# Optimization experiments

Hardware: AMD Instinct MI355X
Metric: run time of the kernel (lower is better)

## Reference

```python
import jax, jax.numpy as jnp
import numpy as np

HEADS = 8
HDIM = 64
MAX_PEMB = 512


def setup_inputs() -> dict:
    key = jax.random.key(0)
    ks = jax.random.split(key, 6)
    B, S, D = 4, 1024, 512
    return {
        "x": jax.random.normal(ks[0], (B, S, D), jnp.float32),
        "attn_mask": jnp.ones((B, S), jnp.bool_),
        "Wq": jax.random.normal(ks[1], (D, HEADS * HDIM), jnp.float32) * 0.02,
        "Wkv": jax.random.normal(ks[2], (D, 2 * HEADS * HDIM), jnp.float32) * 0.02,
        "Wout": jax.random.normal(ks[3], (HEADS * HDIM, D), jnp.float32) * 0.02,
        "bout": jnp.zeros((D,), jnp.float32),
        "pemb": jax.random.normal(ks[4], (2 * MAX_PEMB + 1, HDIM), jnp.float32) * 0.02,
    }


def reference(x, attn_mask, Wq, Wkv, Wout, bout, pemb):
    # attn_mask is unpacked but unused in the original call(); faithful to source.
    B, S, D = x.shape
    scale = HDIM ** (-0.5)

    q = (x @ Wq).reshape(B, S, HEADS, HDIM).transpose(0, 2, 1, 3)  # [B,H,S,hd]
    kv = x @ Wkv
    k, v = jnp.split(kv, 2, axis=-1)
    k = k.reshape(B, S, HEADS, HDIM).transpose(0, 2, 1, 3)
    v = v.reshape(B, S, HEADS, HDIM).transpose(0, 2, 1, 3)

    attn_score = jnp.einsum('bhqd,bhkd->bhqk', q, k) * scale

    seq = jnp.arange(S)
    dist = jnp.clip(seq[:, None] - seq[None, :], -MAX_PEMB, MAX_PEMB) + MAX_PEMB  # [S,S]
    rel_pemb = pemb[dist]  # [S,S,hd]
    pos_attn = jnp.einsum('bhsd,std->bhst', q, rel_pemb) * scale  # [B,H,S,S]

    attn_probs = jax.nn.softmax(attn_score + pos_attn, axis=-1)
    ctx = jnp.einsum('bhqk,bhkd->bqhd', attn_probs, v).reshape(B, S, HEADS * HDIM)
    return ctx @ Wout + bout
```

## Files before the change

kernel.cpp:

```cpp
#include <hip/hip_runtime.h>
#include <hip/hip_bf16.h>

constexpr int BATCH = 4;
constexpr int SEQ   = 1024;
constexpr int DM    = 512;
constexpr int NH    = 8;
constexpr int HD    = 64;
constexpr int NQKV  = 1536;

typedef unsigned short u16;
typedef __attribute__((ext_vector_type(8))) __bf16 bf8;
typedef __attribute__((ext_vector_type(4))) __bf16 bf4;
typedef __attribute__((ext_vector_type(4))) float  f4;
typedef __attribute__((ext_vector_type(16))) float f16v;

#define MFMA16(a, b, c) __builtin_amdgcn_mfma_f32_16x16x32_bf16(a, b, c, 0, 0, 0)
#define MFMA32(a, b, c) __builtin_amdgcn_mfma_f32_32x32x16_bf16(a, b, c, 0, 0, 0)

#define QSC 0.18033688f

static __device__ __forceinline__ u16 f2b(float f) {
    union { float f; unsigned u; } v; v.f = f;
    unsigned r = v.u + 0x7FFFu + ((v.u >> 16) & 1u);
    return (u16)(r >> 16);
}
static __device__ __forceinline__ float b2f(u16 x) {
    union { unsigned u; float f; } v; v.u = (unsigned)x << 16;
    return v.f;
}
static __device__ __forceinline__ float fexp2(float x) {
    return __builtin_amdgcn_exp2f(x);
}
static __device__ __forceinline__ void gl_lds16(const void* g, void* l) {
    __builtin_amdgcn_global_load_lds(
        (const __attribute__((address_space(1))) void*)g,
        (__attribute__((address_space(3))) void*)l, 16, 0, 0);
}
static __device__ __forceinline__ unsigned cvtpk_bf16(float lo, float hi) {
    unsigned r;
    asm("v_cvt_pk_bf16_f32 %0, %1, %2" : "=v"(r) : "v"(lo), "v"(hi));
    return r;
}
static __device__ __forceinline__ void swap32(unsigned &a, unsigned &b) {
    asm("v_permlane32_swap_b32 %0, %1" : "+v"(a), "+v"(b));
}

__device__ __forceinline__ void tcvt_tile(const float* __restrict__ in,
                                          u16* __restrict__ out,
                                          int R, int C, int bx, int by, int tid,
                                          float (*t)[33]) {
    int r0 = by * 32, c0 = bx * 32;
    int lc = tid & 31, lr = tid >> 5;
    #pragma unroll
    for (int p = 0; p < 4; p++) {
        int r = lr + p * 8;
        t[r][lc] = in[(size_t)(r0 + r) * C + c0 + lc];
    }
    __syncthreads();
    #pragma unroll
    for (int p = 0; p < 4; p++) {
        int r = lr + p * 8;
        out[(size_t)(c0 + r) * R + r0 + lc] = f2b(t[lc][r]);
    }
}

__global__ __launch_bounds__(256)
void prep(const float* __restrict__ x, const float* __restrict__ Wq,
          const float* __restrict__ Wkv, const float* __restrict__ Wout,
          const float* __restrict__ pemb,
          u16* __restrict__ xb, u16* __restrict__ qkvw,
          u16* __restrict__ Woutt, u16* __restrict__ pembb) {
    __shared__ float t[32][33];
    const int blk = blockIdx.x, tid = threadIdx.x;
    if (blk < 2048) {
        int i = (blk * 256 + tid) * 4;
        float4 v = *(const float4*)(x + i);
        ushort4 o = {f2b(v.x), f2b(v.y), f2b(v.z), f2b(v.w)};
        *(ushort4*)(xb + i) = o;
    } else if (blk < 2113) {
        int i = ((blk - 2048) * 256 + tid) * 4;
        if (i < 1025 * HD) {
            float4 v = *(const float4*)(pemb + i);
            ushort4 o = {f2b(v.x), f2b(v.y), f2b(v.z), f2b(v.w)};
            *(ushort4*)(pembb + i) = o;
        }
    } else if (blk < 2369) {
        int l = blk - 2113;
        tcvt_tile(Wq, qkvw, 512, 512, l & 15, l >> 4, tid, t);
    } else if (blk < 2881) {
        int l = blk - 2369;
        tcvt_tile(Wkv, qkvw + 512 * 512, 512, 1024, l & 31, l >> 5, tid, t);
    } else {
        int l = blk - 2881;
        tcvt_tile(Wout, Woutt, 512, 512, l & 15, l >> 4, tid, t);
    }
}

template<int BN>
__global__ __launch_bounds__(256)
void gemm_bt(const u16* __restrict__ A, const u16* __restrict__ Bt,
             int M, int N, int K,
             float* __restrict__ Cf, const float* __restrict__ bias,
             __bf16* __restrict__ qtb, __bf16* __restrict__ ktb,
             __bf16* __restrict__ vtb) {
    constexpr int NJ = BN / 32;
    __shared__ __align__(16) u16 As[2][64][32];
    __shared__ __align__(16) u16 Bs[2][BN][32];
    const int tid = threadIdx.x, w = tid >> 6, lane = tid & 63;
    const int l15 = lane & 15, l4 = lane >> 4;
    const int wr = (w >> 1) * 32, wc = (w & 1) * (BN / 2);
    const int bm = blockIdx.y * 64, bn = blockIdx.x * BN;

    f4 acc[2][NJ];
    #pragma unroll
    for (int i = 0; i < 2; i++)
        #pragma unroll
        for (int j = 0; j < NJ; j++) acc[i][j] = (f4){0.f, 0.f, 0.f, 0.f};

    const int rS = lane >> 2;
    const int cS = (lane & 3) * 8;

    for (int k0 = 0; k0 < K; k0 += 64) {
        #pragma unroll
        for (int ks = 0; ks < 2; ks++) {
            gl_lds16(A + (size_t)(bm + w * 16 + rS) * K + k0 + ks * 32 + cS,
                     &As[ks][w * 16][0]);
            #pragma unroll
            for (int rb = 0; rb < BN / 4; rb += 16)
                gl_lds16(Bt + (size_t)(bn + w * (BN / 4) + rb + rS) * K
                             + k0 + ks * 32 + cS,
                         &Bs[ks][w * (BN / 4) + rb][0]);
        }
        __syncthreads();
        #pragma unroll
        for (int ks = 0; ks < 2; ks++) {
            bf8 af[2], bf[NJ];
            #pragma unroll
            for (int i = 0; i < 2; i++)
                af[i] = *(const bf8*)&As[ks][wr + i * 16 + l15][l4 * 8];
            #pragma unroll
            for (int j = 0; j < NJ; j++)
                bf[j] = *(const bf8*)&Bs[ks][wc + j * 16 + l15][l4 * 8];
            #pragma unroll
            for (int i = 0; i < 2; i++)
                #pragma unroll
                for (int j = 0; j < NJ; j++)
                    acc[i][j] = MFMA16(af[i], bf[j], acc[i][j]);
        }
        __syncthreads();
    }
    #pragma unroll
    for (int i = 0; i < 2; i++)
        #pragma unroll
        for (int j = 0; j < NJ; j++) {
            const int col = bn + wc + j * 16 + l15;
            const int row0 = bm + wr + i * 16 + l4 * 4;
            if (Cf) {
                #pragma unroll
                for (int reg = 0; reg < 4; reg++)
                    Cf[(size_t)(row0 + reg) * N + col] = acc[i][j][reg] + bias[col];
            } else if (col < 512) {
                int h = col >> 6, d = col & 63;
                #pragma unroll
                for (int reg = 0; reg < 4; reg++) {
                    int row = row0 + reg;
                    int b = row >> 10, t = row & 1023;
                    qtb[((((size_t)(b * 8 + h)) << 10 | t) << 6) | d] =
                        (__bf16)(acc[i][j][reg] * QSC);
                }
            } else if (col < 1024) {
                int h = (col >> 6) - 8, d = col & 63;
                #pragma unroll
                for (int reg = 0; reg < 4; reg++) {
                    int row = row0 + reg;
                    int b = row >> 10, t = row & 1023;
                    ktb[((((size_t)(b * 8 + h)) << 10 | t) << 6) | d] =
                        (__bf16)acc[i][j][reg];
                }
            } else {
                int h = (col >> 6) - 16, d = col & 63;
                int b = row0 >> 10, t = row0 & 1023;
                __bf16 pk[4];
                #pragma unroll
                for (int reg = 0; reg < 4; reg++) pk[reg] = (__bf16)acc[i][j][reg];
                *(ushort4*)&vtb[(((size_t)(b * 8 + h) * 64 + d) << 10) | t] =
                    *(ushort4*)pk;
            }
        }
}

__global__ __launch_bounds__(256)
void attn_mfma(const u16* __restrict__ qtb, const u16* __restrict__ ktb,
               const u16* __restrict__ vtb, const u16* __restrict__ pembb,
               __bf16* __restrict__ ctxb) {
    __shared__ __align__(16) __bf16 Kb[2][64][72];
    __shared__ __align__(16) __bf16 Vb[2][64][72];
    __shared__ __align__(16) __bf16 Qd[256][72];

    const int tid = threadIdx.x, w = tid >> 6, lane = tid & 63;
    const int l31 = lane & 31, hi = lane >> 5;
    const int wq = w >> 1, wt = w & 1;
    const int bh = blockIdx.x, b = bh >> 3;
    const int s0 = blockIdx.y * 64;

    bf8 qb[4];
    {
        const u16* qp = qtb + ((size_t)bh * SEQ + s0 + wq * 32 + l31) * HD + hi * 8;
        #pragma unroll
        for (int st = 0; st < 4; st++) qb[st] = *(const bf8*)(qp + st * 16);
    }

    #pragma unroll
    for (int pass = 0; pass < 2; pass++) {
        const int jr = s0 + 449 + pass * 64 + wt * 32 + l31;
        const int jc = min(1024, max(0, jr));
        const u16* pp = pembb + (size_t)jc * HD + hi * 8;
        f16v acc;
        #pragma unroll
        for (int r = 0; r < 16; r++) acc[r] = 0.f;
        #pragma unroll
        for (int st = 0; st < 4; st++) {
            bf8 pj = *(const bf8*)(pp + st * 16);
            acc = MFMA32(qb[st], pj, acc);
        }
        #pragma unroll
        for (int o4 = 0; o4 < 4; o4++) {
            bf4 pk;
            #pragma unroll
            for (int r = 0; r < 4; r++) pk[r] = (__bf16)acc[o4 * 4 + r];
            *(bf4*)&Qd[jr & 255][wq * 32 + o4 * 8 + hi * 4] = pk;
        }
    }

    float l_lane = 0.f;
    f16v oo[2];
    #pragma unroll
    for (int dt = 0; dt < 2; dt++)
        #pragma unroll
        for (int r = 0; r < 16; r++) oo[dt][r] = 0.f;

    const u16* kbase = ktb + (size_t)bh * SEQ * HD;
    const u16* vbase = vtb + (size_t)bh * HD * SEQ;
    const int sr = tid >> 3, sc = (tid & 7) * 8;

    *(bf8*)&Kb[0][sr][sc]      = *(const bf8*)(kbase + (size_t)sr * HD + sc);
    *(bf8*)&Kb[0][sr + 32][sc] = *(const bf8*)(kbase + (size_t)(sr + 32) * HD + sc);
    *(bf8*)&Vb[0][sr][sc]      = *(const bf8*)(vbase + (size_t)sr * SEQ + sc);
    *(bf8*)&Vb[0][sr + 32][sc] = *(const bf8*)(vbase + (size_t)(sr + 32) * SEQ + sc);
    __syncthreads();

    for (int i = 0; i < 16; i++) {
        const int cur = i & 1, nxt = cur ^ 1;
        const int t0 = i * 64, t1 = t0 + 64;
        const bool pre = (i < 15);
        bf8 kr0, kr1, vr0, vr1, pj0, pj1, pj2, pj3;
        const int jrn = s0 + 449 - 64 * (i + 1) + wt * 32 + l31;
        if (pre) {
            kr0 = *(const bf8*)(kbase + (size_t)(t1 + sr) * HD + sc);
            kr1 = *(const bf8*)(kbase + (size_t)(t1 + sr + 32) * HD + sc);
            vr0 = *(const bf8*)(vbase + (size_t)sr * SEQ + t1 + sc);
            vr1 = *(const bf8*)(vbase + (size_t)(sr + 32) * SEQ + t1 + sc);
            const int jc = min(1024, max(0, jrn));
            const u16* pp = pembb + (size_t)jc * HD + hi * 8;
            pj0 = *(const bf8*)(pp);
            pj1 = *(const bf8*)(pp + 16);
            pj2 = *(const bf8*)(pp + 32);
            pj3 = *(const bf8*)(pp + 48);
        }

        bf8 ka[4];
        #pragma unroll
        for (int st = 0; st < 4; st++)
            ka[st] = *(const bf8*)&Kb[cur][wt * 32 + l31][st * 16 + hi * 8];
        const int jcst = (s0 - t0 + 512) + wq * 32 + l31 - wt * 32 - 4 * hi;
        const u16* qdc = (const u16*)&Qd[0][0] + wq * 32 + l31;
        u16 rg[16];
        #pragma unroll
        for (int r = 0; r < 16; r++) {
            const int pat = (r & 3) + 8 * (r >> 2);
            rg[r] = qdc[((jcst - pat) & 255) * 72];
        }
        bf8 vf00 = *(const bf8*)&Vb[cur][l31][wt * 32 + hi * 8];
        bf8 vf01 = *(const bf8*)&Vb[cur][l31][wt * 32 + 16 + hi * 8];
        bf8 vf10 = *(const bf8*)&Vb[cur][32 + l31][wt * 32 + hi * 8];
        bf8 vf11 = *(const bf8*)&Vb[cur][32 + l31][wt * 32 + 16 + hi * 8];

        __builtin_amdgcn_s_setprio(1);
        f16v s16;
        #pragma unroll
        for (int r = 0; r < 16; r++) s16[r] = 0.f;
        #pragma unroll
        for (int st = 0; st < 4; st++) s16 = MFMA32(ka[st], qb[st], s16);
        __builtin_amdgcn_s_setprio(0);

        float p[16];
        float la = 0.f, lb = 0.f;
        #pragma unroll
        for (int r = 0; r < 8; r++) {
            float pv = fexp2(s16[r] + b2f(rg[r]));
            p[r] = pv; la += pv;
        }
        unsigned w00 = cvtpk_bf16(p[0], p[1]), w01 = cvtpk_bf16(p[2], p[3]);
        unsigned w10 = cvtpk_bf16(p[4], p[5]), w11 = cvtpk_bf16(p[6], p[7]);
        swap32(w00, w10); swap32(w01, w11);
        union { unsigned u[4]; bf8 v; } pa0, pa1;
        pa0.u[0] = w00; pa0.u[1] = w01; pa0.u[2] = w10; pa0.u[3] = w11;
        __builtin_amdgcn_s_setprio(1);
        oo[0] = MFMA32(pa0.v, vf00, oo[0]);
        oo[1] = MFMA32(pa0.v, vf10, oo[1]);
        __builtin_amdgcn_s_setprio(0);

        if (pre) {
            *(bf8*)&Kb[nxt][sr][sc]      = kr0;
            *(bf8*)&Kb[nxt][sr + 32][sc] = kr1;
            *(bf8*)&Vb[nxt][sr][sc]      = vr0;
            *(bf8*)&Vb[nxt][sr + 32][sc] = vr1;
        }
        f16v rf;
        if (pre) {
            #pragma unroll
            for (int r = 0; r < 16; r++) rf[r] = 0.f;
            rf = MFMA32(qb[0], pj0, rf);
            rf = MFMA32(qb[1], pj1, rf);
            rf = MFMA32(qb[2], pj2, rf);
            rf = MFMA32(qb[3], pj3, rf);
        }

        #pragma unroll
        for (int r = 8; r < 16; r++) {
            float pv = fexp2(s16[r] + b2f(rg[r]));
            p[r] = pv; lb += pv;
        }
        unsigned w20 = cvtpk_bf16(p[8],  p[9]),  w21 = cvtpk_bf16(p[10], p[11]);
        unsigned w30 = cvtpk_bf16(p[12], p[13]), w31 = cvtpk_bf16(p[14], p[15]);
        swap32(w20, w30); swap32(w21, w31);
        pa1.u[0] = w20; pa1.u[1] = w21; pa1.u[2] = w30; pa1.u[3] = w31;
        __builtin_amdgcn_s_setprio(1);
        oo[0] = MFMA32(pa1.v, vf01, oo[0]);
        oo[1] = MFMA32(pa1.v, vf11, oo[1]);
        __builtin_amdgcn_s_setprio(0);
        l_lane += la + lb;

        if (pre) {
            #pragma unroll
            for (int o4 = 0; o4 < 4; o4++) {
                bf4 pk;
                #pragma unroll
                for (int r = 0; r < 4; r++) pk[r] = (__bf16)rf[o4 * 4 + r];
                *(bf4*)&Qd[jrn & 255][wq * 32 + o4 * 8 + hi * 4] = pk;
            }
        }
        __syncthreads();
    }

    float lsum = l_lane + __shfl_xor(l_lane, 32);
    float* Os = (float*)&Qd[0][0];
    float* Ls = Os + 4096;
    if (lane < 32) Ls[(wq * 2 + wt) * 32 + l31] = lsum;
    if (wt == 0) {
        #pragma unroll
        for (int dt = 0; dt < 2; dt++)
            #pragma unroll
            for (int r = 0; r < 16; r++) {
                const int q = (r & 3) + 8 * (r >> 2) + 4 * hi;
                Os[(wq * 32 + q) * 64 + dt * 32 + l31] = oo[dt][r];
            }
    }
    __syncthreads();
    if (wt == 1) {
        const int h = bh & 7;
        #pragma unroll
        for (int r = 0; r < 16; r++) {
            const int q = (r & 3) + 8 * (r >> 2) + 4 * hi;
            const float li = 1.f / (Ls[wq * 64 + q] + Ls[wq * 64 + 32 + q]);
            #pragma unroll
            for (int dt = 0; dt < 2; dt++) {
                float v = (oo[dt][r] + Os[(wq * 32 + q) * 64 + dt * 32 + l31]) * li;
                ctxb[(size_t)(b * SEQ + s0 + wq * 32 + q) * DM + h * HD + dt * 32 + l31]
                    = (__bf16)v;
            }
        }
    }
}

extern "C" void kernel_launch(void* const* d_in, const int* in_sizes, int n_in,
                              void* d_out, int out_size, void* d_ws, size_t ws_size,
                              hipStream_t stream) {
    const float* x    = (const float*)d_in[0];
    const float* Wq   = (const float*)d_in[2];
    const float* Wkv  = (const float*)d_in[3];
    const float* Wout = (const float*)d_in[4];
    const float* bout = (const float*)d_in[5];
    const float* pemb = (const float*)d_in[6];
    float* out = (float*)d_out;

    const int M = BATCH * SEQ;
    u16* p = (u16*)d_ws;
    u16* xb    = p; p += (size_t)M * DM;
    u16* qkvw  = p; p += (size_t)NQKV * DM;
    u16* Woutt = p; p += (size_t)DM * DM;
    u16* pembb = p; p += (size_t)1025 * HD;
    u16* qtb   = p; p += (size_t)M * DM;
    u16* ktb   = p; p += (size_t)M * DM;
    u16* vtb   = p; p += (size_t)M * DM;
    u16* ctxb  = p; p += (size_t)M * DM;

    prep<<<3137, 256, 0, stream>>>(x, Wq, Wkv, Wout, pemb, xb, qkvw, Woutt, pembb);

    gemm_bt<128><<<dim3(NQKV / 128, M / 64), 256, 0, stream>>>(
        xb, qkvw, M, NQKV, DM, nullptr, nullptr,
        (__bf16*)qtb, (__bf16*)ktb, (__bf16*)vtb);

    attn_mfma<<<dim3(BATCH * NH, SEQ / 64), 256, 0, stream>>>(
        qtb, ktb, vtb, pembb, (__bf16*)ctxb);

    gemm_bt<64><<<dim3(DM / 64, M / 64), 256, 0, stream>>>(
        ctxb, Woutt, M, DM, DM, out, bout, nullptr, nullptr, nullptr);
}
```

Measured before the change: 124.7 us.

## Load K/V MFMA fragments directly from global into registers, drop LDS staging

Removes the shared-memory double buffers for K and V. Each lane now loads its MFMA operand fragments straight from global memory into a two-deep register prefetch buffer, and the main loop is fully unrolled so the register indices stay static. This cuts LDS writes and reads and the bank traffic for K/V. In exchange, each K/V element is fetched by both waves that share a wt half, and register pressure rises.

```diff
diff --git a/kernel.cpp b/kernel.cpp
--- a/kernel.cpp
+++ b/kernel.cpp
@@ -193,8 +193,6 @@
 void attn_mfma(const u16* __restrict__ qtb, const u16* __restrict__ ktb,
                const u16* __restrict__ vtb, const u16* __restrict__ pembb,
                __bf16* __restrict__ ctxb) {
-    __shared__ __align__(16) __bf16 Kb[2][64][72];
-    __shared__ __align__(16) __bf16 Vb[2][64][72];
     __shared__ __align__(16) __bf16 Qd[256][72];
 
     const int tid = threadIdx.x, w = tid >> 6, lane = tid & 63;
@@ -210,6 +208,20 @@
         for (int st = 0; st < 4; st++) qb[st] = *(const bf8*)(qp + st * 16);
     }
 
+    const u16* kbase = ktb + (size_t)bh * SEQ * HD;
+    const u16* vbase = vtb + (size_t)bh * HD * SEQ;
+    const u16* kp  = kbase + (size_t)(wt * 32 + l31) * HD + hi * 8;
+    const u16* vp0 = vbase + (size_t)l31 * SEQ        + wt * 32 + hi * 8;
+    const u16* vp1 = vbase + (size_t)(32 + l31) * SEQ + wt * 32 + hi * 8;
+
+    bf8 kf[2][4], vf[2][4];
+    #pragma unroll
+    for (int st = 0; st < 4; st++) kf[0][st] = *(const bf8*)(kp + st * 16);
+    vf[0][0] = *(const bf8*)(vp0);
+    vf[0][1] = *(const bf8*)(vp0 + 16);
+    vf[0][2] = *(const bf8*)(vp1);
+    vf[0][3] = *(const bf8*)(vp1 + 16);
+
     #pragma unroll
     for (int pass = 0; pass < 2; pass++) {
         const int jr = s0 + 449 + pass * 64 + wt * 32 + l31;
@@ -239,39 +251,32 @@
         #pragma unroll
         for (int r = 0; r < 16; r++) oo[dt][r] = 0.f;
 
-    const u16* kbase = ktb + (size_t)bh * SEQ * HD;
-    const u16* vbase = vtb + (size_t)bh * HD * SEQ;
-    const int sr = tid >> 3, sc = (tid & 7) * 8;
-
-    *(bf8*)&Kb[0][sr][sc]      = *(const bf8*)(kbase + (size_t)sr * HD + sc);
-    *(bf8*)&Kb[0][sr + 32][sc] = *(const bf8*)(kbase + (size_t)(sr + 32) * HD + sc);
-    *(bf8*)&Vb[0][sr][sc]      = *(const bf8*)(vbase + (size_t)sr * SEQ + sc);
-    *(bf8*)&Vb[0][sr + 32][sc] = *(const bf8*)(vbase + (size_t)(sr + 32) * SEQ + sc);
     __syncthreads();
 
+    #pragma unroll
     for (int i = 0; i < 16; i++) {
         const int cur = i & 1, nxt = cur ^ 1;
         const int t0 = i * 64, t1 = t0 + 64;
         const bool pre = (i < 15);
-        bf8 kr0, kr1, vr0, vr1, pj0, pj1, pj2, pj3;
+        bf8 pj0, pj1, pj2, pj3;
         const int jrn = s0 + 449 - 64 * (i + 1) + wt * 32 + l31;
         if (pre) {
-            kr0 = *(const bf8*)(kbase + (size_t)(t1 + sr) * HD + sc);
-            kr1 = *(const bf8*)(kbase + (size_t)(t1 + sr + 32) * HD + sc);
-            vr0 = *(const bf8*)(vbase + (size_t)sr * SEQ + t1 + sc);
-            vr1 = *(const bf8*)(vbase + (size_t)(sr + 32) * SEQ + t1 + sc);
             const int jc = min(1024, max(0, jrn));
             const u16* pp = pembb + (size_t)jc * HD + hi * 8;
             pj0 = *(const bf8*)(pp);
             pj1 = *(const bf8*)(pp + 16);
             pj2 = *(const bf8*)(pp + 32);
             pj3 = *(const bf8*)(pp + 48);
-        }
-
-        bf8 ka[4];
-        #pragma unroll
-        for (int st = 0; st < 4; st++)
-            ka[st] = *(const bf8*)&Kb[cur][wt * 32 + l31][st * 16 + hi * 8];
+            kf[nxt][0] = *(const bf8*)(kp + (size_t)t1 * HD);
+            kf[nxt][1] = *(const bf8*)(kp + (size_t)t1 * HD + 16);
+            kf[nxt][2] = *(const bf8*)(kp + (size_t)t1 * HD + 32);
+            kf[nxt][3] = *(const bf8*)(kp + (size_t)t1 * HD + 48);
+            vf[nxt][0] = *(const bf8*)(vp0 + t1);
+            vf[nxt][1] = *(const bf8*)(vp0 + t1 + 16);
+            vf[nxt][2] = *(const bf8*)(vp1 + t1);
+            vf[nxt][3] = *(const bf8*)(vp1 + t1 + 16);
+        }
+
         const int jcst = (s0 - t0 + 512) + wq * 32 + l31 - wt * 32 - 4 * hi;
         const u16* qdc = (const u16*)&Qd[0][0] + wq * 32 + l31;
         u16 rg[16];
@@ -280,17 +285,15 @@
             const int pat = (r & 3) + 8 * (r >> 2);
             rg[r] = qdc[((jcst - pat) & 255) * 72];
         }
-        bf8 vf00 = *(const bf8*)&Vb[cur][l31][wt * 32 + hi * 8];
-        bf8 vf01 = *(const bf8*)&Vb[cur][l31][wt * 32 + 16 + hi * 8];
-        bf8 vf10 = *(const bf8*)&Vb[cur][32 + l31][wt * 32 + hi * 8];
-        bf8 vf11 = *(const bf8*)&Vb[cur][32 + l31][wt * 32 + 16 + hi * 8];
 
         __builtin_amdgcn_s_setprio(1);
         f16v s16;
         #pragma unroll
         for (int r = 0; r < 16; r++) s16[r] = 0.f;
-        #pragma unroll
-        for (int st = 0; st < 4; st++) s16 = MFMA32(ka[st], qb[st], s16);
+        s16 = MFMA32(kf[cur][0], qb[0], s16);
+        s16 = MFMA32(kf[cur][1], qb[1], s16);
+        s16 = MFMA32(kf[cur][2], qb[2], s16);
+        s16 = MFMA32(kf[cur][3], qb[3], s16);
         __builtin_amdgcn_s_setprio(0);
 
         float p[16];
@@ -306,16 +309,10 @@
         union { unsigned u[4]; bf8 v; } pa0, pa1;
         pa0.u[0] = w00; pa0.u[1] = w01; pa0.u[2] = w10; pa0.u[3] = w11;
         __builtin_amdgcn_s_setprio(1);
-        oo[0] = MFMA32(pa0.v, vf00, oo[0]);
-        oo[1] = MFMA32(pa0.v, vf10, oo[1]);
+        oo[0] = MFMA32(pa0.v, vf[cur][0], oo[0]);
+        oo[1] = MFMA32(pa0.v, vf[cur][2], oo[1]);
         __builtin_amdgcn_s_setprio(0);
 
-        if (pre) {
-            *(bf8*)&Kb[nxt][sr][sc]      = kr0;
-            *(bf8*)&Kb[nxt][sr + 32][sc] = kr1;
-            *(bf8*)&Vb[nxt][sr][sc]      = vr0;
-            *(bf8*)&Vb[nxt][sr + 32][sc] = vr1;
-        }
         f16v rf;
         if (pre) {
             #pragma unroll
@@ -336,8 +333,8 @@
         swap32(w20, w30); swap32(w21, w31);
         pa1.u[0] = w20; pa1.u[1] = w21; pa1.u[2] = w30; pa1.u[3] = w31;
         __builtin_amdgcn_s_setprio(1);
-        oo[0] = MFMA32(pa1.v, vf01, oo[0]);
-        oo[1] = MFMA32(pa1.v, vf11, oo[1]);
+        oo[0] = MFMA32(pa1.v, vf[cur][1], oo[0]);
+        oo[1] = MFMA32(pa1.v, vf[cur][3], oo[1]);
         __builtin_amdgcn_s_setprio(0);
         l_lane += la + lb;
 
```

After: 143.3 us. +15.0%, slower.
